# Kernel optimization log

Hardware: AMD Instinct MI355X
Metric: run time of the kernel (lower is better)

## Reference

```python
import jax, jax.numpy as jnp
import numpy as np

N, K, D_LOCAL, P, BINS = 8192, 32, 256, 128, 64
N_RBF, REL_CLIP = 16, 32
REL_DIM = 2 * REL_CLIP + 2  # 65 rel-pos buckets + 1 'different chain/batch' bucket
N_ATOMS = 5


def _normalize(v, eps=1e-8):
    return v / (jnp.linalg.norm(v, axis=-1, keepdims=True) + eps)


def _frames(pos):
    # Gram-Schmidt backbone frames from N, CA, C atoms. pos: [N, A, 3]
    n, ca, c = pos[:, 0], pos[:, 1], pos[:, 2]
    e1 = _normalize(c - ca)
    v2 = n - ca
    e2 = _normalize(v2 - jnp.sum(v2 * e1, -1, keepdims=True) * e1)
    e3 = jnp.cross(e1, e2)
    return jnp.stack([e1, e2, e3], axis=-1)  # [N, 3, 3], columns are basis


def setup_inputs() -> dict:
    key = jax.random.key(0)
    ks = jax.random.split(key, 16)
    inp = {
        "local": jax.random.normal(ks[0], (N, D_LOCAL), jnp.float32),
        "pos": jax.random.normal(ks[1], (N, N_ATOMS, 3), jnp.float32) * 3.0,
        "neighbours": jax.random.randint(ks[2], (N, K), 0, N, jnp.int32),
        "resi": jnp.arange(N, dtype=jnp.int32),
        "chain": jnp.zeros((N,), jnp.int32),
        "batch": jnp.zeros((N,), jnp.int32),
        "mask": jnp.ones((N,), bool),
    }
    def lin(k, fan_in, fan_out):
        return jax.random.normal(k, (fan_in, fan_out), jnp.float32) / np.sqrt(fan_in)
    inp["W_relpos"] = lin(ks[3], REL_DIM, P)
    inp["W_dist"] = lin(ks[4], N_RBF, P)
    inp["W_dir"] = lin(ks[5], 3, P)
    inp["W_rot"] = lin(ks[6], 9, P)
    inp["W_pvec"] = lin(ks[7], N_ATOMS * 3, P)
    inp["W_loc_i"] = lin(ks[8], D_LOCAL, P)
    inp["W_loc_j"] = lin(ks[9], D_LOCAL, P)
    inp["ln_scale"] = jnp.ones((P,), jnp.float32)
    inp["ln_bias"] = jnp.zeros((P,), jnp.float32)
    inp["W1"] = lin(ks[10], P, 2 * P)
    inp["b1"] = jnp.zeros((2 * P,), jnp.float32)
    inp["W2"] = lin(ks[11], 2 * P, BINS) * 0.02  # final layer (small init; zeros in original)
    inp["b2"] = jnp.zeros((BINS,), jnp.float32)
    return inp


def reference(local, pos, neighbours, resi, chain, batch, mask,
              W_relpos, W_dist, W_dir, W_rot, W_pvec, W_loc_i, W_loc_j,
              ln_scale, ln_bias, W1, b1, W2, b2):
    idx = jnp.where(neighbours < 0, 0, neighbours)          # safe gather index [N, K]
    m = mask.astype(jnp.float32)
    pair_mask = m[:, None] * m[idx] * (neighbours != -1)    # [N, K]

    # --- sequence relative position (one-hot, clipped to +/-32) ---
    rel = jnp.clip(resi[idx] - resi[:, None], -REL_CLIP, REL_CLIP) + REL_CLIP
    same = (chain[:, None] == chain[idx]) & (batch[:, None] == batch[idx])
    code = jnp.where(same, rel, REL_DIM - 1)
    f_rel = jax.nn.one_hot(code, REL_DIM, dtype=jnp.float32)  # [N, K, 66]

    # --- geometric features ---
    ca = pos[:, 1]                                           # [N, 3]
    R = _frames(pos)                                         # [N, 3, 3]
    dvec = ca[idx] - ca[:, None]                             # [N, K, 3]
    d = jnp.linalg.norm(dvec, axis=-1)                       # [N, K]
    centers = jnp.linspace(0.0, 22.0, N_RBF)
    sigma = 22.0 / N_RBF
    f_dist = jnp.exp(-((d[..., None] - centers) ** 2) / (2 * sigma ** 2))  # [N,K,16]
    unit = dvec / (d[..., None] + 1e-8)
    f_dir = jnp.einsum("nab,nka->nkb", R, unit)              # [N, K, 3] direction in local frame
    f_rot = jnp.einsum("nab,nkac->nkbc", R, R[idx]).reshape(d.shape + (9,))  # R_i^T R_j
    pv = pos[idx] - ca[:, None, None]                        # [N, K, A, 3]
    f_pv = jnp.einsum("nab,nkma->nkmb", R, pv).reshape(d.shape + (N_ATOMS * 3,))

    # --- multi-branch linear fusion ---
    pair = (f_rel @ W_relpos + f_dist @ W_dist + f_dir @ W_dir
            + f_rot @ W_rot + f_pv @ W_pvec
            + (local @ W_loc_i)[:, None] + (local @ W_loc_j)[idx])
    pair = pair * pair_mask[..., None]

    # --- LayerNorm (create_scale/offset, eps=1e-5) ---
    mu = jnp.mean(pair, axis=-1, keepdims=True)
    var = jnp.mean((pair - mu) ** 2, axis=-1, keepdims=True)
    pair = (pair - mu) * jax.lax.rsqrt(var + 1e-5) * ln_scale + ln_bias

    # --- MLP + log_softmax ---
    hidden = jax.nn.gelu(pair @ W1 + b1)
    distogram = hidden @ W2 + b2                             # [N, K, 64]
    return jax.nn.log_softmax(distogram, axis=-1)
```

## Files before the change

kernel.cpp:

```cpp
#include <hip/hip_runtime.h>
#include <hip/hip_bf16.h>
#include <math.h>

#define N_NODES 8192
#define KNBR    32
#define PDIM    128
#define BINS    64
#define REL_CLIP 32
#define REL_DIM  66
#define RSTR    136

typedef unsigned short ushort_t;
typedef short v8s  __attribute__((ext_vector_type(8)));
typedef float v4f  __attribute__((ext_vector_type(4)));

__device__ __forceinline__ ushort_t f2bf(float f) {
    union { __hip_bfloat16 b; ushort_t u; } cv;
    cv.b = __float2bfloat16(f);
    return cv.u;
}
__device__ __forceinline__ unsigned int pk2bf(float lo, float hiv) {
    union { __hip_bfloat162 h2; unsigned int u; } cv;
    cv.h2 = __float22bfloat162_rn(make_float2(lo, hiv));
    return cv.u;
}
__device__ __forceinline__ float gelu_sig(float x) {
    float e = exp2f(-2.4554045f * x);
    return x / (1.f + e);
}

__global__ __launch_bounds__(256) void prep_kernel(
    const float* __restrict__ W_dist, const float* __restrict__ W_dir,
    const float* __restrict__ W_rot, const float* __restrict__ W_pvec,
    const float* __restrict__ W_relpos,
    const float* __restrict__ W1, const float* __restrict__ W2,
    const float* __restrict__ W_loc_i, const float* __restrict__ W_loc_j,
    const float* __restrict__ ln_scale, const float* __restrict__ ln_bias,
    const float* __restrict__ b1,
    ushort_t* __restrict__ Wcomb, ushort_t* __restrict__ W1Ts,
    ushort_t* __restrict__ W2T, ushort_t* __restrict__ W_locT,
    float* __restrict__ b1p)
{
    int idx = blockIdx.x * 256 + threadIdx.x;
    if (idx < 16384) {
        int col = idx >> 7, k = idx & 127;
        float v = 0.f;
        if (k < 16)       v = W_dist[k * PDIM + col];
        else if (k < 19)  v = W_dir[(k - 16) * PDIM + col];
        else if (k < 28)  v = W_rot[(k - 19) * PDIM + col];
        else if (k < 43)  v = W_pvec[(k - 28) * PDIM + col];
        else if (k < 109) v = W_relpos[(size_t)(k - 43) * PDIM + col];
        Wcomb[idx] = f2bf(v);
    } else if (idx < 49152) {
        int o = idx - 16384;
        int col = o >> 7, k = o & 127;
        W1Ts[o] = f2bf(W1[(size_t)k * 256 + col] * ln_scale[k]);
    } else if (idx < 65536) {
        int o = idx - 49152;
        int col = o >> 8, k = o & 255;
        W2T[o] = f2bf(W2[(size_t)k * BINS + col]);
    } else if (idx < 131072) {
        int o = idx - 65536;
        int oc = o >> 8, k = o & 255;
        float v = (oc < 128) ? W_loc_i[(size_t)k * 128 + oc]
                             : W_loc_j[(size_t)k * 128 + (oc - 128)];
        W_locT[o] = f2bf(v);
    } else if (idx < 131328) {
        int c = idx - 131072;
        float s = b1[c];
        for (int k = 0; k < 128; ++k) s += ln_bias[k] * W1[(size_t)k * 256 + c];
        b1p[c] = s;
    }
}

__global__ __launch_bounds__(256) void locframe_kernel(
    const float* __restrict__ local, const float* __restrict__ pos,
    const ushort_t* __restrict__ W_locT,
    float* __restrict__ R_ws, float* __restrict__ loci_ws, float* __restrict__ locj_ws)
{
    __shared__ __align__(16) ushort_t LB[32 * 264];
    const int tid = threadIdx.x;
    const int base = blockIdx.x * 32;
    const int wid = tid >> 6, lane = tid & 63, c15 = lane & 15, hi = lane >> 4;

    if (tid < 32) {
        const int n = base + tid;
        const float* pp = pos + (size_t)n * 15;
        float nx = pp[0], ny = pp[1], nz = pp[2];
        float cax = pp[3], cay = pp[4], caz = pp[5];
        float cx = pp[6], cy = pp[7], cz = pp[8];
        float e1x = cx - cax, e1y = cy - cay, e1z = cz - caz;
        float n1 = sqrtf(e1x*e1x + e1y*e1y + e1z*e1z) + 1e-8f;
        e1x /= n1; e1y /= n1; e1z /= n1;
        float v2x = nx - cax, v2y = ny - cay, v2z = nz - caz;
        float dp = v2x*e1x + v2y*e1y + v2z*e1z;
        float wx = v2x - dp*e1x, wy = v2y - dp*e1y, wz = v2z - dp*e1z;
        float n2 = sqrtf(wx*wx + wy*wy + wz*wz) + 1e-8f;
        float e2x = wx/n2, e2y = wy/n2, e2z = wz/n2;
        float4 f0, f1, f2;
        f0.x = e1x; f0.y = e1y; f0.z = e1z; f0.w = e2x;
        f1.x = e2y; f1.y = e2z;
        f1.z = e1y*e2z - e1z*e2y;
        f1.w = e1z*e2x - e1x*e2z;
        f2.x = e1x*e2y - e1y*e2x;
        f2.y = 0.f; f2.z = 0.f; f2.w = 0.f;
        float* R = R_ws + (size_t)n * 12;
        *(float4*)&R[0] = f0;
        *(float4*)&R[4] = f1;
        *(float4*)&R[8] = f2;
    }
    #pragma unroll
    for (int it = 0; it < 8; ++it) {
        int f = tid + it * 256;
        int row = f >> 6, kc = f & 63;
        float4 L = *(const float4*)&local[((size_t)(base + row)) * 256 + kc * 4];
        uint2 w8; w8.x = pk2bf(L.x, L.y); w8.y = pk2bf(L.z, L.w);
        *(uint2*)&LB[row * 264 + kc * 4] = w8;
    }
    __syncthreads();

    v4f acc[4][2];
    #pragma unroll
    for (int a = 0; a < 4; ++a)
        #pragma unroll
        for (int b = 0; b < 2; ++b) { acc[a][b][0]=0.f; acc[a][b][1]=0.f; acc[a][b][2]=0.f; acc[a][b][3]=0.f; }
    #pragma unroll
    for (int ks = 0; ks < 8; ++ks) {
        v8s bF[2];
        #pragma unroll
        for (int bt = 0; bt < 2; ++bt)
            bF[bt] = *(const v8s*)&LB[(bt*16 + c15) * 264 + ks*32 + hi*8];
        #pragma unroll
        for (int act = 0; act < 4; ++act) {
            v8s aF = *(const v8s*)&W_locT[(size_t)(wid*64 + act*16 + c15) * 256 + ks*32 + hi*8];
            #pragma unroll
            for (int bt = 0; bt < 2; ++bt)
                acc[act][bt] = __builtin_amdgcn_mfma_f32_16x16x32_bf16(aF, bF[bt], acc[act][bt], 0, 0, 0);
        }
    }
    #pragma unroll
    for (int act = 0; act < 4; ++act) {
        const int oc0 = wid*64 + act*16 + hi*4;
        #pragma unroll
        for (int bt = 0; bt < 2; ++bt) {
            const int lrow = bt*16 + c15;
            float4 v;
            v.x = acc[act][bt][0]; v.y = acc[act][bt][1];
            v.z = acc[act][bt][2]; v.w = acc[act][bt][3];
            if (oc0 < 128)
                *(float4*)&loci_ws[(size_t)(base + lrow) * 128 + oc0] = v;
            else
                *(float4*)&locj_ws[(size_t)(base + lrow) * 128 + (oc0 - 128)] = v;
        }
    }
}

__device__ __forceinline__ void loadR(const float* __restrict__ R_ws, int n, float* Ri) {
    float4 f0 = *(const float4*)&R_ws[(size_t)n * 12 + 0];
    float4 f1 = *(const float4*)&R_ws[(size_t)n * 12 + 4];
    float4 f2 = *(const float4*)&R_ws[(size_t)n * 12 + 8];
    Ri[0] = f0.x; Ri[1] = f0.y; Ri[2] = f0.z;
    Ri[3] = f0.w; Ri[4] = f1.x; Ri[5] = f1.y;
    Ri[6] = f1.z; Ri[7] = f1.w; Ri[8] = f2.x;
}

__global__ __launch_bounds__(256, 4) void pair_kernel(
    const float* __restrict__ pos, const int* __restrict__ neighbours,
    const int* __restrict__ resi, const int* __restrict__ chain,
    const int* __restrict__ batch, const int* __restrict__ mask,
    const float* __restrict__ b1p, const float* __restrict__ b2,
    const float* __restrict__ R_ws, const float* __restrict__ loci_ws,
    const float* __restrict__ locj_ws,
    const ushort_t* __restrict__ Wcomb, const ushort_t* __restrict__ W1Ts,
    const ushort_t* __restrict__ W2T, float* __restrict__ out)
{
    __shared__ __align__(16) ushort_t SH0[64 * RSTR];
    __shared__ __align__(16) ushort_t HT[64 * RSTR];
    float2* redLN = (float2*)HT;
    float*  redSM = (float*)SH0;

    const int tid = threadIdx.x;
    const int ib = blockIdx.x;
    const int base = ib * 2;
    const int wid = tid >> 6, lane = tid & 63, c15 = lane & 15, hi = lane >> 4;

    int nbv[4], jv[4];
    #pragma unroll
    for (int bt = 0; bt < 4; ++bt) {
        const int rr = bt * 16 + c15;
        nbv[bt] = neighbours[(size_t)(base + (bt >> 1)) * KNBR + (rr & 31)];
        jv[bt] = nbv[bt] < 0 ? 0 : nbv[bt];
    }

    {
        const int row = lane;
        const int node = base + (row >> 5);
        const int nb_f = neighbours[(size_t)node * KNBR + (row & 31)];
        const int jf = nb_f < 0 ? 0 : nb_f;
        const float cax = pos[(size_t)node*15 + 3], cay = pos[(size_t)node*15 + 4], caz = pos[(size_t)node*15 + 5];
        const float* pj = pos + (size_t)jf * 15;
        const float dx = pj[3] - cax, dy = pj[4] - cay, dz = pj[5] - caz;
        ushort_t* fr = &SH0[row * RSTR];
        float Ri[9];

        #define DOTR(b,X,Y,Z) (Ri[(b)*3]*(X) + Ri[(b)*3+1]*(Y) + Ri[(b)*3+2]*(Z))
        if (wid == 0) {
            const float d = sqrtf(dx*dx + dy*dy + dz*dz);
            v8s v0, v1;
            #pragma unroll
            for (int r = 0; r < 8; ++r) {
                float a0 = d - (22.f/15.f)*r;        v0[r] = (short)f2bf(__expf(-a0*a0*(1.f/3.78125f)));
                float a1 = d - (22.f/15.f)*(r + 8);  v1[r] = (short)f2bf(__expf(-a1*a1*(1.f/3.78125f)));
            }
            *(v8s*)&fr[0] = v0;
            *(v8s*)&fr[8] = v1;
        } else if (wid == 1) {
            loadR(R_ws, node, Ri);
            float Rj[9];
            loadR(R_ws, jf, Rj);
            const float d = sqrtf(dx*dx + dy*dy + dz*dz);
            const float inv = 1.f / (d + 1e-8f);
            const float ux = dx*inv, uy = dy*inv, uz = dz*inv;
            #define ROT(b,c) (Ri[(b)*3]*Rj[(c)*3] + Ri[(b)*3+1]*Rj[(c)*3+1] + Ri[(b)*3+2]*Rj[(c)*3+2])
            const float p0x = pj[0]-cax, p0y = pj[1]-cay, p0z = pj[2]-caz;
            v8s v0, v1;
            v0[0] = (short)f2bf(DOTR(0, ux, uy, uz));
            v0[1] = (short)f2bf(DOTR(1, ux, uy, uz));
            v0[2] = (short)f2bf(DOTR(2, ux, uy, uz));
            v0[3] = (short)f2bf(ROT(0,0));
            v0[4] = (short)f2bf(ROT(0,1));
            v0[5] = (short)f2bf(ROT(0,2));
            v0[6] = (short)f2bf(ROT(1,0));
            v0[7] = (short)f2bf(ROT(1,1));
            v1[0] = (short)f2bf(ROT(1,2));
            v1[1] = (short)f2bf(ROT(2,0));
            v1[2] = (short)f2bf(ROT(2,1));
            v1[3] = (short)f2bf(ROT(2,2));
            v1[4] = (short)f2bf(DOTR(0, p0x, p0y, p0z));
            v1[5] = (short)f2bf(DOTR(1, p0x, p0y, p0z));
            v1[6] = (short)f2bf(DOTR(2, p0x, p0y, p0z));
            v1[7] = (short)f2bf(DOTR(0, dx, dy, dz));
            *(v8s*)&fr[16] = v0;
            *(v8s*)&fr[24] = v1;
            #undef ROT
        } else if (wid == 2) {
            loadR(R_ws, node, Ri);
            const float p2x = pj[6]-cax, p2y = pj[7]-cay, p2z = pj[8]-caz;
            const float p3x = pj[9]-cax, p3y = pj[10]-cay, p3z = pj[11]-caz;
            v8s v;
            v[0] = (short)f2bf(DOTR(1, dx, dy, dz));
            v[1] = (short)f2bf(DOTR(2, dx, dy, dz));
            v[2] = (short)f2bf(DOTR(0, p2x, p2y, p2z));
            v[3] = (short)f2bf(DOTR(1, p2x, p2y, p2z));
            v[4] = (short)f2bf(DOTR(2, p2x, p2y, p2z));
            v[5] = (short)f2bf(DOTR(0, p3x, p3y, p3z));
            v[6] = (short)f2bf(DOTR(1, p3x, p3y, p3z));
            v[7] = (short)f2bf(DOTR(2, p3x, p3y, p3z));
            *(v8s*)&fr[32] = v;
        } else {
            loadR(R_ws, node, Ri);
            const float p4x = pj[12]-cax, p4y = pj[13]-cay, p4z = pj[14]-caz;
            v8s v = {0,0,0,0,0,0,0,0};
            v[0] = (short)f2bf(DOTR(0, p4x, p4y, p4z));
            v[1] = (short)f2bf(DOTR(1, p4x, p4y, p4z));
            v[2] = (short)f2bf(DOTR(2, p4x, p4y, p4z));
            *(v8s*)&fr[40] = v;
            const v8s z = {0,0,0,0,0,0,0,0};
            #pragma unroll
            for (int c = 6; c < 16; ++c) *(v8s*)&fr[c * 8] = z;
            int rel = resi[jf] - resi[node];
            rel = rel < -REL_CLIP ? -REL_CLIP : (rel > REL_CLIP ? REL_CLIP : rel);
            rel += REL_CLIP;
            const int code = ((chain[jf] == chain[node]) && (batch[jf] == batch[node])) ? rel : (REL_DIM - 1);
            fr[43 + code] = (ushort_t)0x3F80;
        }
        #undef DOTR
    }
    __syncthreads();

    float mu0, mu1, mu2, mu3, rs0, rs1, rs2, rs3;
    {
        v4f pacc[2][4];
        #pragma unroll
        for (int at = 0; at < 2; ++at)
            #pragma unroll
            for (int bt = 0; bt < 4; ++bt) { pacc[at][bt][0]=0.f; pacc[at][bt][1]=0.f; pacc[at][bt][2]=0.f; pacc[at][bt][3]=0.f; }
        #pragma unroll
        for (int ks = 0; ks < 4; ++ks) {
            v8s bF[4];
            #pragma unroll
            for (int bt = 0; bt < 4; ++bt)
                bF[bt] = *(const v8s*)&SH0[(bt*16 + c15) * RSTR + (ks*4 + hi) * 8];
            #pragma unroll
            for (int at = 0; at < 2; ++at) {
                v8s aF = *(const v8s*)&Wcomb[(size_t)((wid*2 + at)*16 + c15) * 128 + ks*32 + hi*8];
                #pragma unroll
                for (int bt = 0; bt < 4; ++bt)
                    pacc[at][bt] = __builtin_amdgcn_mfma_f32_16x16x32_bf16(aF, bF[bt], pacc[at][bt], 0, 0, 0);
            }
        }
        const int mi0 = mask[base], mi1 = mask[base + 1];
        float pmv[4];
        #pragma unroll
        for (int bt = 0; bt < 4; ++bt) {
            const int min_ = (bt < 2) ? mi0 : mi1;
            pmv[bt] = (min_ != 0 && mask[jv[bt]] != 0 && nbv[bt] != -1) ? 1.f : 0.f;
        }
        float4 liA[2][2], ljA[2][4];
        #pragma unroll
        for (int at = 0; at < 2; ++at) {
            const int ch0 = wid*32 + at*16 + hi*4;
            liA[at][0] = *(const float4*)&loci_ws[(size_t)base * 128 + ch0];
            liA[at][1] = *(const float4*)&loci_ws[(size_t)(base + 1) * 128 + ch0];
            #pragma unroll
            for (int bt = 0; bt < 4; ++bt)
                ljA[at][bt] = *(const float4*)&locj_ws[(size_t)jv[bt] * 128 + ch0];
        }
        float sA[4], qA[4];
        #pragma unroll
        for (int bt = 0; bt < 4; ++bt) {
            float s = 0.f, q = 0.f;
            #pragma unroll
            for (int at = 0; at < 2; ++at) {
                const float4 li = (bt < 2) ? liA[at][0] : liA[at][1];
                const float4 lj = ljA[at][bt];
                float v0 = (pacc[at][bt][0] + li.x + lj.x) * pmv[bt];
                float v1 = (pacc[at][bt][1] + li.y + lj.y) * pmv[bt];
                float v2 = (pacc[at][bt][2] + li.z + lj.z) * pmv[bt];
                float v3 = (pacc[at][bt][3] + li.w + lj.w) * pmv[bt];
                pacc[at][bt][0] = v0; pacc[at][bt][1] = v1; pacc[at][bt][2] = v2; pacc[at][bt][3] = v3;
                s += v0 + v1 + v2 + v3;
                q += v0*v0 + v1*v1 + v2*v2 + v3*v3;
            }
            s += __shfl_xor(s, 16, 64);  q += __shfl_xor(q, 16, 64);
            s += __shfl_xor(s, 32, 64);  q += __shfl_xor(q, 32, 64);
            sA[bt] = s; qA[bt] = q;
        }
        {
            float ssel = hi == 0 ? sA[0] : hi == 1 ? sA[1] : hi == 2 ? sA[2] : sA[3];
            float qsel = hi == 0 ? qA[0] : hi == 1 ? qA[1] : hi == 2 ? qA[2] : qA[3];
            redLN[lane * 5 + wid] = make_float2(ssel, qsel);
        }
        __syncthreads();
        #pragma unroll
        for (int bt = 0; bt < 4; ++bt) {
            const int rr = bt*16 + c15;
            float2 r0 = redLN[rr*5+0], r1 = redLN[rr*5+1], r2 = redLN[rr*5+2], r3 = redLN[rr*5+3];
            float s = r0.x + r1.x + r2.x + r3.x;
            float q = r0.y + r1.y + r2.y + r3.y;
            float mu = s * (1.f/128.f);
            float rs = rsqrtf(q * (1.f/128.f) - mu*mu + 1e-5f);
            if (bt == 0) { mu0 = mu; rs0 = rs; }
            else if (bt == 1) { mu1 = mu; rs1 = rs; }
            else if (bt == 2) { mu2 = mu; rs2 = rs; }
            else { mu3 = mu; rs3 = rs; }
        }
        #pragma unroll
        for (int at = 0; at < 2; ++at) {
            const int chA = wid*4 + at*2 + (hi >> 1);
            #pragma unroll
            for (int bt = 0; bt < 4; ++bt) {
                const float mu = bt == 0 ? mu0 : bt == 1 ? mu1 : bt == 2 ? mu2 : mu3;
                const float rs = bt == 0 ? rs0 : bt == 1 ? rs1 : bt == 2 ? rs2 : rs3;
                const float nm = -mu * rs;
                float z0 = fmaf(pacc[at][bt][0], rs, nm);
                float z1 = fmaf(pacc[at][bt][1], rs, nm);
                float z2 = fmaf(pacc[at][bt][2], rs, nm);
                float z3 = fmaf(pacc[at][bt][3], rs, nm);
                uint2 w8; w8.x = pk2bf(z0, z1); w8.y = pk2bf(z2, z3);
                const int row = bt*16 + c15;
                *(uint2*)&SH0[row * RSTR + chA * 8 + (hi & 1) * 4] = w8;
            }
        }
    }
    __syncthreads();

    v4f acc5[4];
    #pragma unroll
    for (int bt = 0; bt < 4; ++bt) { acc5[bt][0]=0.f; acc5[bt][1]=0.f; acc5[bt][2]=0.f; acc5[bt][3]=0.f; }
    #pragma unroll
    for (int half = 0; half < 2; ++half) {
        v4f acc4[2][4];
        #pragma unroll
        for (int at = 0; at < 2; ++at)
            #pragma unroll
            for (int bt = 0; bt < 4; ++bt) { acc4[at][bt][0]=0.f; acc4[at][bt][1]=0.f; acc4[at][bt][2]=0.f; acc4[at][bt][3]=0.f; }
        #pragma unroll
        for (int ks = 0; ks < 4; ++ks) {
            v8s bF[4];
            #pragma unroll
            for (int bt = 0; bt < 4; ++bt)
                bF[bt] = *(const v8s*)&SH0[(bt*16 + c15) * RSTR + (ks*4 + hi) * 8];
            #pragma unroll
            for (int at = 0; at < 2; ++at) {
                v8s aF = *(const v8s*)&W1Ts[(size_t)(half*128 + wid*32 + at*16 + c15) * 128 + ks*32 + hi*8];
                #pragma unroll
                for (int bt = 0; bt < 4; ++bt)
                    acc4[at][bt] = __builtin_amdgcn_mfma_f32_16x16x32_bf16(aF, bF[bt], acc4[at][bt], 0, 0, 0);
            }
        }
        #pragma unroll
        for (int at = 0; at < 2; ++at) {
            const int h0 = half*128 + wid*32 + at*16 + hi*4;
            const float4 bv = *(const float4*)&b1p[h0];
            const int chA = wid*4 + at*2 + (hi >> 1);
            #pragma unroll
            for (int bt = 0; bt < 4; ++bt) {
                float g0 = gelu_sig(acc4[at][bt][0] + bv.x);
                float g1 = gelu_sig(acc4[at][bt][1] + bv.y);
                float g2 = gelu_sig(acc4[at][bt][2] + bv.z);
                float g3 = gelu_sig(acc4[at][bt][3] + bv.w);
                uint2 w8; w8.x = pk2bf(g0, g1); w8.y = pk2bf(g2, g3);
                const int row = bt*16 + c15;
                *(uint2*)&HT[row * RSTR + chA * 8 + (hi & 1) * 4] = w8;
            }
        }
        __syncthreads();
        #pragma unroll
        for (int ks = 0; ks < 4; ++ks) {
            v8s aF = *(const v8s*)&W2T[(size_t)(wid*16 + c15) * 256 + half*128 + ks*32 + hi*8];
            #pragma unroll
            for (int bt = 0; bt < 4; ++bt) {
                v8s bF = *(const v8s*)&HT[(bt*16 + c15) * RSTR + (ks*4 + hi) * 8];
                acc5[bt] = __builtin_amdgcn_mfma_f32_16x16x32_bf16(aF, bF, acc5[bt], 0, 0, 0);
            }
        }
        if (half == 0) __syncthreads();
    }

    {
        const float4 bv = *(const float4*)&b2[wid*16 + hi*4];
        float sW[4];
        #pragma unroll
        for (int bt = 0; bt < 4; ++bt) {
            acc5[bt][0] += bv.x; acc5[bt][1] += bv.y; acc5[bt][2] += bv.z; acc5[bt][3] += bv.w;
            float s = __expf(acc5[bt][0]) + __expf(acc5[bt][1])
                    + __expf(acc5[bt][2]) + __expf(acc5[bt][3]);
            s += __shfl_xor(s, 16, 64);
            s += __shfl_xor(s, 32, 64);
            sW[bt] = s;
        }
        {
            float ssel = hi == 0 ? sW[0] : hi == 1 ? sW[1] : hi == 2 ? sW[2] : sW[3];
            redSM[lane * 5 + wid] = ssel;
        }
        __syncthreads();
        #pragma unroll
        for (int bt = 0; bt < 4; ++bt) {
            const int rr = bt*16 + c15;
            float S = redSM[rr*5+0] + redSM[rr*5+1] + redSM[rr*5+2] + redSM[rr*5+3];
            const float lz = __logf(S);
            float4 o;
            o.x = acc5[bt][0] - lz; o.y = acc5[bt][1] - lz;
            o.z = acc5[bt][2] - lz; o.w = acc5[bt][3] - lz;
            *(float4*)&out[((size_t)(ib * 64 + rr)) * 64 + wid*16 + hi*4] = o;
        }
    }
}

extern "C" void kernel_launch(void* const* d_in, const int* in_sizes, int n_in,
                              void* d_out, int out_size, void* d_ws, size_t ws_size,
                              hipStream_t stream) {
    (void)in_sizes; (void)n_in; (void)out_size; (void)ws_size;
    const float* local   = (const float*)d_in[0];
    const float* pos     = (const float*)d_in[1];
    const int* neighbours= (const int*)d_in[2];
    const int* resi      = (const int*)d_in[3];
    const int* chain     = (const int*)d_in[4];
    const int* batch     = (const int*)d_in[5];
    const int* mask      = (const int*)d_in[6];
    const float* W_relpos= (const float*)d_in[7];
    const float* W_dist  = (const float*)d_in[8];
    const float* W_dir   = (const float*)d_in[9];
    const float* W_rot   = (const float*)d_in[10];
    const float* W_pvec  = (const float*)d_in[11];
    const float* W_loc_i = (const float*)d_in[12];
    const float* W_loc_j = (const float*)d_in[13];
    const float* ln_scale= (const float*)d_in[14];
    const float* ln_bias = (const float*)d_in[15];
    const float* W1      = (const float*)d_in[16];
    const float* b1      = (const float*)d_in[17];
    const float* W2      = (const float*)d_in[18];
    const float* b2      = (const float*)d_in[19];
    float* out = (float*)d_out;

    float* R_ws    = (float*)d_ws;
    float* loci_ws = R_ws + (size_t)N_NODES * 12;
    float* locj_ws = loci_ws + (size_t)N_NODES * PDIM;
    ushort_t* Wcomb = (ushort_t*)(locj_ws + (size_t)N_NODES * PDIM);
    ushort_t* W1Ts  = Wcomb + 16384;
    ushort_t* W2T   = W1Ts + 32768;
    ushort_t* W_locT= W2T + 16384;
    float* b1p      = (float*)(W_locT + 65536);

    hipLaunchKernelGGL(prep_kernel, dim3(514), dim3(256), 0, stream,
                       W_dist, W_dir, W_rot, W_pvec, W_relpos, W1, W2,
                       W_loc_i, W_loc_j, ln_scale, ln_bias, b1,
                       Wcomb, W1Ts, W2T, W_locT, b1p);
    hipLaunchKernelGGL(locframe_kernel, dim3(N_NODES / 32), dim3(256), 0, stream,
                       local, pos, W_locT, R_ws, loci_ws, locj_ws);
    hipLaunchKernelGGL(pair_kernel, dim3(N_NODES / 2), dim3(256), 0, stream,
                       pos, neighbours, resi, chain, batch, mask, b1p, b2,
                       R_ws, loci_ws, locj_ws, Wcomb, W1Ts, W2T, out);
}
```

Measured before the change: 137.6 us.

## Split pair kernel work across eight waves per block instead of four

Doubles the pair-kernel block to 512 threads. Each wave now owns 16 output channels in the fusion and W1 GEMMs instead of 32, and feature construction (RBF halves, rotation, positions, relpos one-hot, zero fill) is spread over eight waves. The LayerNorm reduction is widened to eight partials, while the final W2 GEMM and softmax run on only four waves. The aim is more latency hiding and less per-wave register pressure. The cost is more barriers per block, idle waves in the last stage, and an aggressive launch bound that may cap registers or cause spills.

Result: slower. 150.7 us (+9.5%).

```diff
diff --git a/kernel.cpp b/kernel.cpp
--- a/kernel.cpp
+++ b/kernel.cpp
@@ -164,7 +164,7 @@
     Ri[6] = f1.z; Ri[7] = f1.w; Ri[8] = f2.x;
 }
 
-__global__ __launch_bounds__(256, 4) void pair_kernel(
+__global__ __launch_bounds__(512, 8) void pair_kernel(
     const float* __restrict__ pos, const int* __restrict__ neighbours,
     const int* __restrict__ resi, const int* __restrict__ chain,
     const int* __restrict__ batch, const int* __restrict__ mask,
@@ -206,15 +206,17 @@
         #define DOTR(b,X,Y,Z) (Ri[(b)*3]*(X) + Ri[(b)*3+1]*(Y) + Ri[(b)*3+2]*(Z))
         if (wid == 0) {
             const float d = sqrtf(dx*dx + dy*dy + dz*dz);
-            v8s v0, v1;
-            #pragma unroll
-            for (int r = 0; r < 8; ++r) {
-                float a0 = d - (22.f/15.f)*r;        v0[r] = (short)f2bf(__expf(-a0*a0*(1.f/3.78125f)));
-                float a1 = d - (22.f/15.f)*(r + 8);  v1[r] = (short)f2bf(__expf(-a1*a1*(1.f/3.78125f)));
-            }
+            v8s v0;
+            #pragma unroll
+            for (int r = 0; r < 8; ++r) { float a0 = d - (22.f/15.f)*r; v0[r] = (short)f2bf(__expf(-a0*a0*(1.f/3.78125f))); }
             *(v8s*)&fr[0] = v0;
+        } else if (wid == 1) {
+            const float d = sqrtf(dx*dx + dy*dy + dz*dz);
+            v8s v1;
+            #pragma unroll
+            for (int r = 0; r < 8; ++r) { float a1 = d - (22.f/15.f)*(r + 8); v1[r] = (short)f2bf(__expf(-a1*a1*(1.f/3.78125f))); }
             *(v8s*)&fr[8] = v1;
-        } else if (wid == 1) {
+        } else if (wid == 2) {
             loadR(R_ws, node, Ri);
             float Rj[9];
             loadR(R_ws, jf, Rj);
@@ -222,8 +224,7 @@
             const float inv = 1.f / (d + 1e-8f);
             const float ux = dx*inv, uy = dy*inv, uz = dz*inv;
             #define ROT(b,c) (Ri[(b)*3]*Rj[(c)*3] + Ri[(b)*3+1]*Rj[(c)*3+1] + Ri[(b)*3+2]*Rj[(c)*3+2])
-            const float p0x = pj[0]-cax, p0y = pj[1]-cay, p0z = pj[2]-caz;
-            v8s v0, v1;
+            v8s v0;
             v0[0] = (short)f2bf(DOTR(0, ux, uy, uz));
             v0[1] = (short)f2bf(DOTR(1, ux, uy, uz));
             v0[2] = (short)f2bf(DOTR(2, ux, uy, uz));
@@ -232,6 +233,15 @@
             v0[5] = (short)f2bf(ROT(0,2));
             v0[6] = (short)f2bf(ROT(1,0));
             v0[7] = (short)f2bf(ROT(1,1));
+            *(v8s*)&fr[16] = v0;
+            #undef ROT
+        } else if (wid == 3) {
+            loadR(R_ws, node, Ri);
+            float Rj[9];
+            loadR(R_ws, jf, Rj);
+            #define ROT(b,c) (Ri[(b)*3]*Rj[(c)*3] + Ri[(b)*3+1]*Rj[(c)*3+1] + Ri[(b)*3+2]*Rj[(c)*3+2])
+            const float p0x = pj[0]-cax, p0y = pj[1]-cay, p0z = pj[2]-caz;
+            v8s v1;
             v1[0] = (short)f2bf(ROT(1,2));
             v1[1] = (short)f2bf(ROT(2,0));
             v1[2] = (short)f2bf(ROT(2,1));
@@ -240,10 +250,9 @@
             v1[5] = (short)f2bf(DOTR(1, p0x, p0y, p0z));
             v1[6] = (short)f2bf(DOTR(2, p0x, p0y, p0z));
             v1[7] = (short)f2bf(DOTR(0, dx, dy, dz));
-            *(v8s*)&fr[16] = v0;
             *(v8s*)&fr[24] = v1;
             #undef ROT
-        } else if (wid == 2) {
+        } else if (wid == 4) {
             loadR(R_ws, node, Ri);
             const float p2x = pj[6]-cax, p2y = pj[7]-cay, p2z = pj[8]-caz;
             const float p3x = pj[9]-cax, p3y = pj[10]-cay, p3z = pj[11]-caz;
@@ -257,22 +266,33 @@
             v[6] = (short)f2bf(DOTR(1, p3x, p3y, p3z));
             v[7] = (short)f2bf(DOTR(2, p3x, p3y, p3z));
             *(v8s*)&fr[32] = v;
-        } else {
+        } else if (wid == 5) {
             loadR(R_ws, node, Ri);
             const float p4x = pj[12]-cax, p4y = pj[13]-cay, p4z = pj[14]-caz;
-            v8s v = {0,0,0,0,0,0,0,0};
-            v[0] = (short)f2bf(DOTR(0, p4x, p4y, p4z));
-            v[1] = (short)f2bf(DOTR(1, p4x, p4y, p4z));
-            v[2] = (short)f2bf(DOTR(2, p4x, p4y, p4z));
-            *(v8s*)&fr[40] = v;
-            const v8s z = {0,0,0,0,0,0,0,0};
-            #pragma unroll
-            for (int c = 6; c < 16; ++c) *(v8s*)&fr[c * 8] = z;
             int rel = resi[jf] - resi[node];
             rel = rel < -REL_CLIP ? -REL_CLIP : (rel > REL_CLIP ? REL_CLIP : rel);
             rel += REL_CLIP;
             const int code = ((chain[jf] == chain[node]) && (batch[jf] == batch[node])) ? rel : (REL_DIM - 1);
-            fr[43 + code] = (ushort_t)0x3F80;
+            v8s v;
+            v[0] = (short)f2bf(DOTR(0, p4x, p4y, p4z));
+            v[1] = (short)f2bf(DOTR(1, p4x, p4y, p4z));
+            v[2] = (short)f2bf(DOTR(2, p4x, p4y, p4z));
+            #pragma unroll
+            for (int t = 3; t < 8; ++t) v[t] = (short)((code == t - 3) ? 0x3F80 : 0);
+            *(v8s*)&fr[40] = v;
+        } else if (wid == 6) {
+            const v8s z = {0,0,0,0,0,0,0,0};
+            *(v8s*)&fr[112] = z;
+            *(v8s*)&fr[120] = z;
+        } else {
+            const v8s z = {0,0,0,0,0,0,0,0};
+            #pragma unroll
+            for (int c = 6; c < 14; ++c) *(v8s*)&fr[c * 8] = z;
+            int rel = resi[jf] - resi[node];
+            rel = rel < -REL_CLIP ? -REL_CLIP : (rel > REL_CLIP ? REL_CLIP : rel);
+            rel += REL_CLIP;
+            const int code = ((chain[jf] == chain[node]) && (batch[jf] == batch[node])) ? rel : (REL_DIM - 1);
+            if (code >= 5) fr[43 + code] = (ushort_t)0x3F80;
         }
         #undef DOTR
     }
@@ -280,58 +300,36 @@
 
     float mu0, mu1, mu2, mu3, rs0, rs1, rs2, rs3;
     {
-        v4f pacc[2][4];
-        #pragma unroll
-        for (int at = 0; at < 2; ++at)
-            #pragma unroll
-            for (int bt = 0; bt < 4; ++bt) { pacc[at][bt][0]=0.f; pacc[at][bt][1]=0.f; pacc[at][bt][2]=0.f; pacc[at][bt][3]=0.f; }
+        v4f pacc[4];
+        #pragma unroll
+        for (int bt = 0; bt < 4; ++bt) { pacc[bt][0]=0.f; pacc[bt][1]=0.f; pacc[bt][2]=0.f; pacc[bt][3]=0.f; }
         #pragma unroll
         for (int ks = 0; ks < 4; ++ks) {
-            v8s bF[4];
-            #pragma unroll
-            for (int bt = 0; bt < 4; ++bt)
-                bF[bt] = *(const v8s*)&SH0[(bt*16 + c15) * RSTR + (ks*4 + hi) * 8];
-            #pragma unroll
-            for (int at = 0; at < 2; ++at) {
-                v8s aF = *(const v8s*)&Wcomb[(size_t)((wid*2 + at)*16 + c15) * 128 + ks*32 + hi*8];
-                #pragma unroll
-                for (int bt = 0; bt < 4; ++bt)
-                    pacc[at][bt] = __builtin_amdgcn_mfma_f32_16x16x32_bf16(aF, bF[bt], pacc[at][bt], 0, 0, 0);
+            v8s aF = *(const v8s*)&Wcomb[(size_t)(wid*16 + c15) * 128 + ks*32 + hi*8];
+            #pragma unroll
+            for (int bt = 0; bt < 4; ++bt) {
+                v8s bF = *(const v8s*)&SH0[(bt*16 + c15) * RSTR + (ks*4 + hi) * 8];
+                pacc[bt] = __builtin_amdgcn_mfma_f32_16x16x32_bf16(aF, bF, pacc[bt], 0, 0, 0);
             }
         }
         const int mi0 = mask[base], mi1 = mask[base + 1];
-        float pmv[4];
+        const int ch0 = wid*16 + hi*4;
+        const float4 li0 = *(const float4*)&loci_ws[(size_t)base * 128 + ch0];
+        const float4 li1 = *(const float4*)&loci_ws[(size_t)(base + 1) * 128 + ch0];
+        float sA[4], qA[4];
         #pragma unroll
         for (int bt = 0; bt < 4; ++bt) {
             const int min_ = (bt < 2) ? mi0 : mi1;
-            pmv[bt] = (min_ != 0 && mask[jv[bt]] != 0 && nbv[bt] != -1) ? 1.f : 0.f;
-        }
-        float4 liA[2][2], ljA[2][4];
-        #pragma unroll
-        for (int at = 0; at < 2; ++at) {
-            const int ch0 = wid*32 + at*16 + hi*4;
-            liA[at][0] = *(const float4*)&loci_ws[(size_t)base * 128 + ch0];
-            liA[at][1] = *(const float4*)&loci_ws[(size_t)(base + 1) * 128 + ch0];
-            #pragma unroll
-            for (int bt = 0; bt < 4; ++bt)
-                ljA[at][bt] = *(const float4*)&locj_ws[(size_t)jv[bt] * 128 + ch0];
-        }
-        float sA[4], qA[4];
-        #pragma unroll
-        for (int bt = 0; bt < 4; ++bt) {
-            float s = 0.f, q = 0.f;
-            #pragma unroll
-            for (int at = 0; at < 2; ++at) {
-                const float4 li = (bt < 2) ? liA[at][0] : liA[at][1];
-                const float4 lj = ljA[at][bt];
-                float v0 = (pacc[at][bt][0] + li.x + lj.x) * pmv[bt];
-                float v1 = (pacc[at][bt][1] + li.y + lj.y) * pmv[bt];
-                float v2 = (pacc[at][bt][2] + li.z + lj.z) * pmv[bt];
-                float v3 = (pacc[at][bt][3] + li.w + lj.w) * pmv[bt];
-                pacc[at][bt][0] = v0; pacc[at][bt][1] = v1; pacc[at][bt][2] = v2; pacc[at][bt][3] = v3;
-                s += v0 + v1 + v2 + v3;
-                q += v0*v0 + v1*v1 + v2*v2 + v3*v3;
-            }
+            const float pm = (min_ != 0 && mask[jv[bt]] != 0 && nbv[bt] != -1) ? 1.f : 0.f;
+            const float4 li = (bt < 2) ? li0 : li1;
+            const float4 lj = *(const float4*)&locj_ws[(size_t)jv[bt] * 128 + ch0];
+            float v0 = (pacc[bt][0] + li.x + lj.x) * pm;
+            float v1 = (pacc[bt][1] + li.y + lj.y) * pm;
+            float v2 = (pacc[bt][2] + li.z + lj.z) * pm;
+            float v3 = (pacc[bt][3] + li.w + lj.w) * pm;
+            pacc[bt][0] = v0; pacc[bt][1] = v1; pacc[bt][2] = v2; pacc[bt][3] = v3;
+            float s = v0 + v1 + v2 + v3;
+            float q = v0*v0 + v1*v1 + v2*v2 + v3*v3;
             s += __shfl_xor(s, 16, 64);  q += __shfl_xor(q, 16, 64);
             s += __shfl_xor(s, 32, 64);  q += __shfl_xor(q, 32, 64);
             sA[bt] = s; qA[bt] = q;
@@ -339,15 +337,18 @@
         {
             float ssel = hi == 0 ? sA[0] : hi == 1 ? sA[1] : hi == 2 ? sA[2] : sA[3];
             float qsel = hi == 0 ? qA[0] : hi == 1 ? qA[1] : hi == 2 ? qA[2] : qA[3];
-            redLN[lane * 5 + wid] = make_float2(ssel, qsel);
+            redLN[lane * 9 + wid] = make_float2(ssel, qsel);
         }
         __syncthreads();
         #pragma unroll
         for (int bt = 0; bt < 4; ++bt) {
             const int rr = bt*16 + c15;
-            float2 r0 = redLN[rr*5+0], r1 = redLN[rr*5+1], r2 = redLN[rr*5+2], r3 = redLN[rr*5+3];
-            float s = r0.x + r1.x + r2.x + r3.x;
-            float q = r0.y + r1.y + r2.y + r3.y;
+            float s = 0.f, q = 0.f;
+            #pragma unroll
+            for (int w = 0; w < 8; ++w) {
+                float2 r = redLN[rr*9 + w];
+                s += r.x; q += r.y;
+            }
             float mu = s * (1.f/128.f);
             float rs = rsqrtf(q * (1.f/128.f) - mu*mu + 1e-5f);
             if (bt == 0) { mu0 = mu; rs0 = rs; }
@@ -355,18 +356,17 @@
             else if (bt == 2) { mu2 = mu; rs2 = rs; }
             else { mu3 = mu; rs3 = rs; }
         }
-        #pragma unroll
-        for (int at = 0; at < 2; ++at) {
-            const int chA = wid*4 + at*2 + (hi >> 1);
+        {
+            const int chA = wid*2 + (hi >> 1);
             #pragma unroll
             for (int bt = 0; bt < 4; ++bt) {
                 const float mu = bt == 0 ? mu0 : bt == 1 ? mu1 : bt == 2 ? mu2 : mu3;
                 const float rs = bt == 0 ? rs0 : bt == 1 ? rs1 : bt == 2 ? rs2 : rs3;
                 const float nm = -mu * rs;
-                float z0 = fmaf(pacc[at][bt][0], rs, nm);
-                float z1 = fmaf(pacc[at][bt][1], rs, nm);
-                float z2 = fmaf(pacc[at][bt][2], rs, nm);
-                float z3 = fmaf(pacc[at][bt][3], rs, nm);
+                float z0 = fmaf(pacc[bt][0], rs, nm);
+                float z1 = fmaf(pacc[bt][1], rs, nm);
+                float z2 = fmaf(pacc[bt][2], rs, nm);
+                float z3 = fmaf(pacc[bt][3], rs, nm);
                 uint2 w8; w8.x = pk2bf(z0, z1); w8.y = pk2bf(z2, z3);
                 const int row = bt*16 + c15;
                 *(uint2*)&SH0[row * RSTR + chA * 8 + (hi & 1) * 4] = w8;
@@ -380,80 +380,76 @@
     for (int bt = 0; bt < 4; ++bt) { acc5[bt][0]=0.f; acc5[bt][1]=0.f; acc5[bt][2]=0.f; acc5[bt][3]=0.f; }
     #pragma unroll
     for (int half = 0; half < 2; ++half) {
-        v4f acc4[2][4];
-        #pragma unroll
-        for (int at = 0; at < 2; ++at)
-            #pragma unroll
-            for (int bt = 0; bt < 4; ++bt) { acc4[at][bt][0]=0.f; acc4[at][bt][1]=0.f; acc4[at][bt][2]=0.f; acc4[at][bt][3]=0.f; }
+        v4f acc4[4];
+        #pragma unroll
+        for (int bt = 0; bt < 4; ++bt) { acc4[bt][0]=0.f; acc4[bt][1]=0.f; acc4[bt][2]=0.f; acc4[bt][3]=0.f; }
         #pragma unroll
         for (int ks = 0; ks < 4; ++ks) {
-            v8s bF[4];
-            #pragma unroll
-            for (int bt = 0; bt < 4; ++bt)
-                bF[bt] = *(const v8s*)&SH0[(bt*16 + c15) * RSTR + (ks*4 + hi) * 8];
-            #pragma unroll
-            for (int at = 0; at < 2; ++at) {
-                v8s aF = *(const v8s*)&W1Ts[(size_t)(half*128 + wid*32 + at*16 + c15) * 128 + ks*32 + hi*8];
-                #pragma unroll
-                for (int bt = 0; bt < 4; ++bt)
-                    acc4[at][bt] = __builtin_amdgcn_mfma_f32_16x16x32_bf16(aF, bF[bt], acc4[at][bt], 0, 0, 0);
-            }
-        }
-        #pragma unroll
-        for (int at = 0; at < 2; ++at) {
-            const int h0 = half*128 + wid*32 + at*16 + hi*4;
+            v8s aF = *(const v8s*)&W1Ts[(size_t)(half*128 + wid*16 + c15) * 128 + ks*32 + hi*8];
+            #pragma unroll
+            for (int bt = 0; bt < 4; ++bt) {
+                v8s bF = *(const v8s*)&SH0[(bt*16 + c15) * RSTR + (ks*4 + hi) * 8];
+                acc4[bt] = __builtin_amdgcn_mfma_f32_16x16x32_bf16(aF, bF, acc4[bt], 0, 0, 0);
+            }
+        }
+        {
+            const int h0 = half*128 + wid*16 + hi*4;
             const float4 bv = *(const float4*)&b1p[h0];
-            const int chA = wid*4 + at*2 + (hi >> 1);
+            const int chA = wid*2 + (hi >> 1);
             #pragma unroll
             for (int bt = 0; bt < 4; ++bt) {
-                float g0 = gelu_sig(acc4[at][bt][0] + bv.x);
-                float g1 = gelu_sig(acc4[at][bt][1] + bv.y);
-                float g2 = gelu_sig(acc4[at][bt][2] + bv.z);
-                float g3 = gelu_sig(acc4[at][bt][3] + bv.w);
+                float g0 = gelu_sig(acc4[bt][0] + bv.x);
+                float g1 = gelu_sig(acc4[bt][1] + bv.y);
+                float g2 = gelu_sig(acc4[bt][2] + bv.z);
+                float g3 = gelu_sig(acc4[bt][3] + bv.w);
                 uint2 w8; w8.x = pk2bf(g0, g1); w8.y = pk2bf(g2, g3);
                 const int row = bt*16 + c15;
                 *(uint2*)&HT[row * RSTR + chA * 8 + (hi & 1) * 4] = w8;
             }
         }
         __syncthreads();
-        #pragma unroll
-        for (int ks = 0; ks < 4; ++ks) {
-            v8s aF = *(const v8s*)&W2T[(size_t)(wid*16 + c15) * 256 + half*128 + ks*32 + hi*8];
+        if (wid < 4) {
+            #pragma unroll
+            for (int ks = 0; ks < 4; ++ks) {
+                v8s aF = *(const v8s*)&W2T[(size_t)(wid*16 + c15) * 256 + half*128 + ks*32 + hi*8];
+                #pragma unroll
+                for (int bt = 0; bt < 4; ++bt) {
+                    v8s bF = *(const v8s*)&HT[(bt*16 + c15) * RSTR + (ks*4 + hi) * 8];
+                    acc5[bt] = __builtin_amdgcn_mfma_f32_16x16x32_bf16(aF, bF, acc5[bt], 0, 0, 0);
+                }
+            }
+        }
+        if (half == 0) __syncthreads();
+    }
+
+    {
+        if (wid < 4) {
+            const float4 bv = *(const float4*)&b2[wid*16 + hi*4];
+            float sW[4];
             #pragma unroll
             for (int bt = 0; bt < 4; ++bt) {
-                v8s bF = *(const v8s*)&HT[(bt*16 + c15) * RSTR + (ks*4 + hi) * 8];
-                acc5[bt] = __builtin_amdgcn_mfma_f32_16x16x32_bf16(aF, bF, acc5[bt], 0, 0, 0);
-            }
-        }
-        if (half == 0) __syncthreads();
-    }
-
-    {
-        const float4 bv = *(const float4*)&b2[wid*16 + hi*4];
-        float sW[4];
-        #pragma unroll
-        for (int bt = 0; bt < 4; ++bt) {
-            acc5[bt][0] += bv.x; acc5[bt][1] += bv.y; acc5[bt][2] += bv.z; acc5[bt][3] += bv.w;
-            float s = __expf(acc5[bt][0]) + __expf(acc5[bt][1])
-                    + __expf(acc5[bt][2]) + __expf(acc5[bt][3]);
-            s += __shfl_xor(s, 16, 64);
-            s += __shfl_xor(s, 32, 64);
-            sW[bt] = s;
-        }
-        {
+                acc5[bt][0] += bv.x; acc5[bt][1] += bv.y; acc5[bt][2] += bv.z; acc5[bt][3] += bv.w;
+                float s = __expf(acc5[bt][0]) + __expf(acc5[bt][1])
+                        + __expf(acc5[bt][2]) + __expf(acc5[bt][3]);
+                s += __shfl_xor(s, 16, 64);
+                s += __shfl_xor(s, 32, 64);
+                sW[bt] = s;
+            }
             float ssel = hi == 0 ? sW[0] : hi == 1 ? sW[1] : hi == 2 ? sW[2] : sW[3];
             redSM[lane * 5 + wid] = ssel;
         }
         __syncthreads();
-        #pragma unroll
-        for (int bt = 0; bt < 4; ++bt) {
-            const int rr = bt*16 + c15;
-            float S = redSM[rr*5+0] + redSM[rr*5+1] + redSM[rr*5+2] + redSM[rr*5+3];
-            const float lz = __logf(S);
-            float4 o;
-            o.x = acc5[bt][0] - lz; o.y = acc5[bt][1] - lz;
-            o.z = acc5[bt][2] - lz; o.w = acc5[bt][3] - lz;
-            *(float4*)&out[((size_t)(ib * 64 + rr)) * 64 + wid*16 + hi*4] = o;
+        if (wid < 4) {
+            #pragma unroll
+            for (int bt = 0; bt < 4; ++bt) {
+                const int rr = bt*16 + c15;
+                float S = redSM[rr*5+0] + redSM[rr*5+1] + redSM[rr*5+2] + redSM[rr*5+3];
+                const float lz = __logf(S);
+                float4 o;
+                o.x = acc5[bt][0] - lz; o.y = acc5[bt][1] - lz;
+                o.z = acc5[bt][2] - lz; o.w = acc5[bt][3] - lz;
+                *(float4*)&out[((size_t)(ib * 64 + rr)) * 64 + wid*16 + hi*4] = o;
+            }
         }
     }
 }
@@ -499,7 +495,7 @@
                        Wcomb, W1Ts, W2T, W_locT, b1p);
     hipLaunchKernelGGL(locframe_kernel, dim3(N_NODES / 32), dim3(256), 0, stream,
                        local, pos, W_locT, R_ws, loci_ws, locj_ws);
-    hipLaunchKernelGGL(pair_kernel, dim3(N_NODES / 2), dim3(256), 0, stream,
+    hipLaunchKernelGGL(pair_kernel, dim3(N_NODES / 2), dim3(512), 0, stream,
                        pos, neighbours, resi, chain, batch, mask, b1p, b2,
                        R_ws, loci_ws, locj_ws, Wcomb, W1Ts, W2T, out);
 }
```
